# Kernel optimization log

Hardware: AMD Instinct MI355X
Metric: run time of the kernel (lower is better)

## Reference

```python
import jax, jax.numpy as jnp
import numpy as np

N, Fdim, Aout = 8192, 32, 8
AVG_DEG = 32.0  # target average degree for the random graph


def setup_inputs() -> dict:
    key = jax.random.key(0)
    ks = jax.random.split(key, 12)
    x = jax.random.normal(ks[0], (N, Fdim), dtype=jnp.float32)
    # binary adjacency, zero diagonal (GCNConv adds self-loops itself)
    u = jax.random.uniform(ks[1], (N, N), dtype=jnp.float32)
    adj = (u < (AVG_DEG / N)).astype(jnp.float32)
    adj = adj * (1.0 - jnp.eye(N, dtype=jnp.float32))
    mask = (jax.random.uniform(ks[2], (N,), dtype=jnp.float32) < 0.5).astype(jnp.float32)

    def lin(k, fout, fin):
        s = 1.0 / np.sqrt(fin)
        return jax.random.uniform(k, (fout, fin), jnp.float32, -s, s)

    return {
        "x": x, "adj": adj, "mask": mask,
        "w1": lin(ks[3], 64, Fdim), "b1": jnp.zeros((64,), jnp.float32),
        "w2": lin(ks[4], 128, 64), "b2": jnp.zeros((128,), jnp.float32),
        "wg": lin(ks[5], 128, 128), "bg": jnp.zeros((128,), jnp.float32),
        "wd": lin(ks[6], 128, 128), "bd": jnp.zeros((128,), jnp.float32),
        "wp1": lin(ks[7], 128, 256), "bp1": jnp.zeros((128,), jnp.float32),
        "wp2": lin(ks[8], 64, 128), "bp2": jnp.zeros((64,), jnp.float32),
        "wo": lin(ks[9], Aout, 64), "bo": jnp.zeros((Aout,), jnp.float32),
    }


def reference(x, adj, mask, w1, b1, w2, b2, wg, bg, wd, bd, wp1, bp1, wp2, bp2, wo, bo):
    # encoder MLP
    h = jax.nn.relu(x @ w1.T + b1)           # [N,64]
    h = jax.nn.relu(h @ w2.T + b2)           # [N,128]
    # GCNConv with default self-loops and symmetric normalization:
    # out = D^{-1/2} (A + I) D^{-1/2} (h W^T) + b
    a_hat = adj + jnp.eye(adj.shape[0], dtype=adj.dtype)
    deg = jnp.sum(a_hat, axis=1)             # >= 1 thanks to self-loops
    dinv = jax.lax.rsqrt(deg)
    msg = h @ wg.T                            # [N,128]
    agg = dinv[:, None] * (a_hat @ (dinv[:, None] * msg))  # normalized aggregation
    g = jax.nn.relu(agg + bg)
    g = jax.nn.relu(g @ wd.T + bd)
    f = jnp.concatenate([g, h], axis=1)       # [N,256]
    p = jax.nn.relu(f @ wp1.T + bp1)
    p = jax.nn.relu(p @ wp2.T + bp2)
    out = (p @ wo.T + bo) * mask[:, None]     # [N,Aout]
    return out
```

## Files before the change

kernel.cpp:

```cpp
#include <hip/hip_runtime.h>

#define N_NODES 8192
#define CAP 128
#define ETILE 16
constexpr int AST = 132;
constexpr int WST = 129;

#define GLDS16(gsrc, ldst)                                                      \
  __builtin_amdgcn_global_load_lds(                                             \
      (const __attribute__((address_space(1))) void*)(gsrc),                    \
      (__attribute__((address_space(3))) void*)(ldst), 16, 0, 0)

__global__ __launch_bounds__(256, 2) void scan_kernel(
    const float* __restrict__ adj, int* __restrict__ cnt,
    int* __restrict__ nbr) {
  __shared__ uint4 stage[4][2][512];
  const int t = threadIdx.x;
  const int lane = t & 63;
  const int w = t >> 6;
  const int row = blockIdx.x * 4 + w;
  const float* rowg = adj + (size_t)row * N_NODES;
  const unsigned long long lmask = (1ull << lane) - 1;

#pragma unroll
  for (int i = 0; i < 8; ++i)
    GLDS16(rowg + i * 256 + lane * 4, &stage[w][0][i * 64]);

  int running = 0;
  int* nbr_row = nbr + (size_t)row * CAP;
#pragma unroll
  for (int ch = 0; ch < 4; ++ch) {
    if (ch < 3) {
#pragma unroll
      for (int i = 0; i < 8; ++i)
        GLDS16(rowg + (ch + 1) * 2048 + i * 256 + lane * 4,
               &stage[w][(ch + 1) & 1][i * 64]);
      __builtin_amdgcn_s_waitcnt(0x3F78);
    } else {
      __builtin_amdgcn_s_waitcnt(0x3F70);
    }
    asm volatile("" ::: "memory");
    uint4 v[8];
#pragma unroll
    for (int i = 0; i < 8; ++i) v[i] = stage[w][ch & 1][i * 64 + lane];
    int c = 0;
#pragma unroll
    for (int i = 0; i < 8; ++i)
      c += (v[i].x != 0u) + (v[i].y != 0u) + (v[i].z != 0u) + (v[i].w != 0u);
    int incl = c;
#pragma unroll
    for (int s = 1; s < 64; s <<= 1) {
      int n = __shfl_up(incl, s);
      if (lane >= s) incl += n;
    }
    int off = running + incl - c;
    running += __shfl(incl, 63);
    const int colbase = ch * 2048;
#pragma unroll
    for (int i = 0; i < 8; ++i) {
      if (v[i].x | v[i].y | v[i].z | v[i].w) {
        const int col = colbase + (i * 64 + lane) * 4;
        if (v[i].x) { if (off < CAP) nbr_row[off] = col + 0; ++off; }
        if (v[i].y) { if (off < CAP) nbr_row[off] = col + 1; ++off; }
        if (v[i].z) { if (off < CAP) nbr_row[off] = col + 2; ++off; }
        if (v[i].w) { if (off < CAP) nbr_row[off] = col + 3; ++off; }
      }
    }
  }
  if (lane == 0) cnt[row] = running;
}

template <int TILE, int K, int KSPLIT, int F, bool RELU, bool BIAS, int SCALEMODE>
__device__ __forceinline__ void layer_op(
    const float (*__restrict__ A0)[AST], const float (*__restrict__ A1)[AST],
    float (*__restrict__ Aout)[AST], float (*__restrict__ Wb)[WST],
    const float* __restrict__ W, const float* __restrict__ bias,
    float* __restrict__ gout, const float* __restrict__ rowscale,
    const int* __restrict__ degcnt, int n0, int t) {
  constexpr int KC = 32;
  constexpr int NCH = K / KC;
  constexpr int ACT = (F * TILE < 256) ? F * TILE : 256;
  constexpr int RS = ACT / F;
  constexpr int RPT = TILE / RS;
  const int c = t % F;
  const int rb = t / F;
  float acc[RPT];
#pragma unroll
  for (int i = 0; i < RPT; ++i) acc[i] = 0.f;

  for (int ch = 0; ch < NCH; ++ch) {
#pragma unroll
    for (int i = 0; i < (F * KC + 255) / 256; ++i) {
      int lin = t + i * 256;
      if ((F * KC) % 256 == 0 || lin < F * KC) {
        int k = lin % KC, f = lin / KC;
        Wb[k][f] = W[(size_t)f * K + ch * KC + k];
      }
    }
    __syncthreads();
    if (t < ACT) {
      const float (*__restrict__ As)[AST] = (ch * KC < KSPLIT) ? A0 : A1;
      const int kb = (ch * KC < KSPLIT) ? ch * KC : ch * KC - KSPLIT;
#pragma unroll
      for (int kg = 0; kg < KC / 4; ++kg) {
        float w0 = Wb[kg * 4 + 0][c];
        float w1v = Wb[kg * 4 + 1][c];
        float w2v = Wb[kg * 4 + 2][c];
        float w3v = Wb[kg * 4 + 3][c];
#pragma unroll
        for (int i = 0; i < RPT; ++i) {
          const float4 a = *(const float4*)&As[rb + i * RS][kb + kg * 4];
          acc[i] = fmaf(a.x, w0, acc[i]);
          acc[i] = fmaf(a.y, w1v, acc[i]);
          acc[i] = fmaf(a.z, w2v, acc[i]);
          acc[i] = fmaf(a.w, w3v, acc[i]);
        }
      }
    }
    __syncthreads();
  }
  if (t < ACT) {
#pragma unroll
    for (int i = 0; i < RPT; ++i) {
      float v = acc[i];
      if (BIAS) v += bias[c];
      if (RELU) v = fmaxf(v, 0.f);
      int node = n0 + rb + i * RS;
      if (SCALEMODE == 1) v *= rowscale[node];
      if (SCALEMODE == 2) v *= rsqrtf((float)degcnt[node] + 1.0f);
      if (Aout) Aout[rb + i * RS][c] = v;
      if (gout) gout[(size_t)node * F + c] = v;
    }
  }
}

__global__ __launch_bounds__(256) void encode_kernel(
    const float* __restrict__ x,
    const float* __restrict__ w1, const float* __restrict__ b1,
    const float* __restrict__ w2, const float* __restrict__ b2,
    const float* __restrict__ wg, const int* __restrict__ cnt,
    float* __restrict__ h_out, float* __restrict__ msg_out) {
  __shared__ float bufA[ETILE][AST];
  __shared__ float bufB[ETILE][AST];
  __shared__ float Wb[32][WST];
  const int t = threadIdx.x;
  const int n0 = blockIdx.x * ETILE;
  if (t < 128) {
    int row = t >> 3, k4 = (t & 7) * 4;
    *(float4*)&bufA[row][k4] = *(const float4*)&x[(size_t)(n0 + row) * 32 + k4];
  }
  layer_op<ETILE, 32, 32, 64, true, true, 0>(bufA, nullptr, bufB, Wb, w1, b1, nullptr, nullptr, nullptr, n0, t);
  layer_op<ETILE, 64, 64, 128, true, true, 0>(bufB, nullptr, bufA, Wb, w2, b2, h_out, nullptr, nullptr, n0, t);
  layer_op<ETILE, 128, 128, 128, false, false, 2>(bufA, nullptr, nullptr, Wb, wg, nullptr, msg_out, nullptr, cnt, n0, t);
}

__global__ __launch_bounds__(256) void agg_kernel(
    const int* __restrict__ cnt, const int* __restrict__ nbr,
    const float* __restrict__ msg, const float* __restrict__ bg,
    const float* __restrict__ adj, float* __restrict__ g1) {
  const int t = threadIdx.x;
  const int f = t & 127;
  const int row = blockIdx.x * 2 + (t >> 7);
  float acc = msg[(size_t)row * 128 + f];
  const int c = cnt[row];
  const float dv = rsqrtf((float)c + 1.0f);
  if (c <= CAP) {
    int i = 0;
    for (; i + 4 <= c; i += 4) {
      int j0 = nbr[(size_t)row * CAP + i + 0];
      int j1 = nbr[(size_t)row * CAP + i + 1];
      int j2 = nbr[(size_t)row * CAP + i + 2];
      int j3 = nbr[(size_t)row * CAP + i + 3];
      float a0 = msg[(size_t)j0 * 128 + f];
      float a1 = msg[(size_t)j1 * 128 + f];
      float a2 = msg[(size_t)j2 * 128 + f];
      float a3 = msg[(size_t)j3 * 128 + f];
      acc += (a0 + a1) + (a2 + a3);
    }
    for (; i < c; ++i) {
      int j = nbr[(size_t)row * CAP + i];
      acc += msg[(size_t)j * 128 + f];
    }
  } else {
    acc = msg[(size_t)row * 128 + f];
    for (int col = 0; col < N_NODES; ++col) {
      if (adj[(size_t)row * N_NODES + col] != 0.f) acc += msg[(size_t)col * 128 + f];
    }
  }
  float v = fmaf(dv, acc, bg[f]);
  g1[(size_t)row * 128 + f] = fmaxf(v, 0.f);
}

__global__ __launch_bounds__(256) void decode_kernel(
    const float* __restrict__ g1, const float* __restrict__ h,
    const float* __restrict__ wd, const float* __restrict__ bd,
    const float* __restrict__ wp1, const float* __restrict__ bp1,
    const float* __restrict__ wp2, const float* __restrict__ bp2,
    const float* __restrict__ wo, const float* __restrict__ bo,
    const float* __restrict__ mask, float* __restrict__ out) {
  __shared__ float bufA[ETILE][AST];
  __shared__ float bufB[ETILE][AST];
  __shared__ float bufH[ETILE][AST];
  __shared__ float Wb[32][WST];
  const int t = threadIdx.x;
  const int n0 = blockIdx.x * ETILE;
#pragma unroll
  for (int i = 0; i < 2; ++i) {
    int lin = t + i * 256;
    int row = lin >> 5, k4 = (lin & 31) * 4;
    *(float4*)&bufA[row][k4] = *(const float4*)&g1[(size_t)(n0 + row) * 128 + k4];
    *(float4*)&bufH[row][k4] = *(const float4*)&h[(size_t)(n0 + row) * 128 + k4];
  }
  layer_op<ETILE, 128, 128, 128, true, true, 0>(bufA, nullptr, bufB, Wb, wd, bd, nullptr, nullptr, nullptr, n0, t);
  layer_op<ETILE, 256, 128, 128, true, true, 0>(bufB, bufH, bufA, Wb, wp1, bp1, nullptr, nullptr, nullptr, n0, t);
  layer_op<ETILE, 128, 128, 64, true, true, 0>(bufA, nullptr, bufB, Wb, wp2, bp2, nullptr, nullptr, nullptr, n0, t);
  layer_op<ETILE, 64, 64, 8, false, true, 1>(bufB, nullptr, nullptr, Wb, wo, bo, out, mask, nullptr, n0, t);
}

extern "C" void kernel_launch(void* const* d_in, const int* in_sizes, int n_in,
                              void* d_out, int out_size, void* d_ws, size_t ws_size,
                              hipStream_t stream) {
  const float* x    = (const float*)d_in[0];
  const float* adj  = (const float*)d_in[1];
  const float* mask = (const float*)d_in[2];
  const float* w1   = (const float*)d_in[3];
  const float* b1   = (const float*)d_in[4];
  const float* w2   = (const float*)d_in[5];
  const float* b2   = (const float*)d_in[6];
  const float* wg   = (const float*)d_in[7];
  const float* bg   = (const float*)d_in[8];
  const float* wd   = (const float*)d_in[9];
  const float* bd   = (const float*)d_in[10];
  const float* wp1  = (const float*)d_in[11];
  const float* bp1  = (const float*)d_in[12];
  const float* wp2  = (const float*)d_in[13];
  const float* bp2  = (const float*)d_in[14];
  const float* wo   = (const float*)d_in[15];
  const float* bo   = (const float*)d_in[16];
  float* out = (float*)d_out;

  float* ws = (float*)d_ws;
  float* h    = ws; ws += (size_t)N_NODES * 128;
  float* msg  = ws; ws += (size_t)N_NODES * 128;
  float* g1   = ws; ws += (size_t)N_NODES * 128;
  int* cnt = (int*)ws; ws += N_NODES;
  int* nbr = (int*)ws;

  scan_kernel<<<N_NODES / 4, 256, 0, stream>>>(adj, cnt, nbr);
  encode_kernel<<<N_NODES / ETILE, 256, 0, stream>>>(x, w1, b1, w2, b2, wg, cnt, h, msg);
  agg_kernel<<<N_NODES / 2, 256, 0, stream>>>(cnt, nbr, msg, bg, adj, g1);
  decode_kernel<<<N_NODES / ETILE, 256, 0, stream>>>(
      g1, h, wd, bd, wp1, bp1, wp2, bp2, wo, bo, mask, out);
}
```

Baseline: 465.2 us.

## Use register-prefetched nontemporal loads in scan, two rows per thread in agg, smaller decode tile

The adjacency scan drops the LDS-staged global_load_lds double buffer. It now prefetches the next chunk straight into registers with nontemporal loads, and the occupancy hint rises to 4 blocks per SM. The aggregation kernel handles two rows per thread with masked, clamped neighbor loads so more independent gathers are in flight, at the cost of some wasted loads when the two degrees differ. The decode kernel uses an 8-row tile, which doubles the block count and cuts LDS use per block but reuses each weight tile less.

```diff
diff --git a/kernel.cpp b/kernel.cpp
--- a/kernel.cpp
+++ b/kernel.cpp
@@ -3,46 +3,30 @@
 #define N_NODES 8192
 #define CAP 128
 #define ETILE 16
+#define DTILE 8
 constexpr int AST = 132;
 constexpr int WST = 129;
 
-#define GLDS16(gsrc, ldst)                                                      \
-  __builtin_amdgcn_global_load_lds(                                             \
-      (const __attribute__((address_space(1))) void*)(gsrc),                    \
-      (__attribute__((address_space(3))) void*)(ldst), 16, 0, 0)
-
-__global__ __launch_bounds__(256, 2) void scan_kernel(
+typedef unsigned u32x4 __attribute__((ext_vector_type(4)));
+
+__global__ __launch_bounds__(256, 4) void scan_kernel(
     const float* __restrict__ adj, int* __restrict__ cnt,
     int* __restrict__ nbr) {
-  __shared__ uint4 stage[4][2][512];
   const int t = threadIdx.x;
   const int lane = t & 63;
-  const int w = t >> 6;
-  const int row = blockIdx.x * 4 + w;
-  const float* rowg = adj + (size_t)row * N_NODES;
-  const unsigned long long lmask = (1ull << lane) - 1;
-
-#pragma unroll
-  for (int i = 0; i < 8; ++i)
-    GLDS16(rowg + i * 256 + lane * 4, &stage[w][0][i * 64]);
-
+  const int row = blockIdx.x * 4 + (t >> 6);
+  const u32x4* rowp = (const u32x4*)(adj + (size_t)row * N_NODES);
+  u32x4 v[8], vn[8];
+#pragma unroll
+  for (int i = 0; i < 8; ++i) v[i] = __builtin_nontemporal_load(&rowp[i * 64 + lane]);
   int running = 0;
   int* nbr_row = nbr + (size_t)row * CAP;
-#pragma unroll
   for (int ch = 0; ch < 4; ++ch) {
     if (ch < 3) {
-#pragma unroll
-      for (int i = 0; i < 8; ++i)
-        GLDS16(rowg + (ch + 1) * 2048 + i * 256 + lane * 4,
-               &stage[w][(ch + 1) & 1][i * 64]);
-      __builtin_amdgcn_s_waitcnt(0x3F78);
-    } else {
-      __builtin_amdgcn_s_waitcnt(0x3F70);
-    }
-    asm volatile("" ::: "memory");
-    uint4 v[8];
-#pragma unroll
-    for (int i = 0; i < 8; ++i) v[i] = stage[w][ch & 1][i * 64 + lane];
+      const u32x4* cp = rowp + (ch + 1) * 512;
+#pragma unroll
+      for (int i = 0; i < 8; ++i) vn[i] = __builtin_nontemporal_load(&cp[i * 64 + lane]);
+    }
     int c = 0;
 #pragma unroll
     for (int i = 0; i < 8; ++i)
@@ -66,6 +50,8 @@
         if (v[i].w) { if (off < CAP) nbr_row[off] = col + 3; ++off; }
       }
     }
+#pragma unroll
+    for (int i = 0; i < 8; ++i) v[i] = vn[i];
   }
   if (lane == 0) cnt[row] = running;
 }
@@ -160,35 +146,39 @@
     const float* __restrict__ adj, float* __restrict__ g1) {
   const int t = threadIdx.x;
   const int f = t & 127;
-  const int row = blockIdx.x * 2 + (t >> 7);
-  float acc = msg[(size_t)row * 128 + f];
-  const int c = cnt[row];
-  const float dv = rsqrtf((float)c + 1.0f);
-  if (c <= CAP) {
-    int i = 0;
-    for (; i + 4 <= c; i += 4) {
-      int j0 = nbr[(size_t)row * CAP + i + 0];
-      int j1 = nbr[(size_t)row * CAP + i + 1];
-      int j2 = nbr[(size_t)row * CAP + i + 2];
-      int j3 = nbr[(size_t)row * CAP + i + 3];
-      float a0 = msg[(size_t)j0 * 128 + f];
-      float a1 = msg[(size_t)j1 * 128 + f];
-      float a2 = msg[(size_t)j2 * 128 + f];
-      float a3 = msg[(size_t)j3 * 128 + f];
-      acc += (a0 + a1) + (a2 + a3);
-    }
-    for (; i < c; ++i) {
-      int j = nbr[(size_t)row * CAP + i];
-      acc += msg[(size_t)j * 128 + f];
+  const int rA = blockIdx.x * 4 + (t >> 7) * 2;
+  const int rB = rA + 1;
+  const int cA = cnt[rA], cB = cnt[rB];
+  float a0 = msg[(size_t)rA * 128 + f];
+  float a1 = msg[(size_t)rB * 128 + f];
+  if (cA <= CAP && cB <= CAP) {
+    const int* nA = nbr + (size_t)rA * CAP;
+    const int* nB = nbr + (size_t)rB * CAP;
+    const int cm = max(cA, cB);
+    for (int i = 0; i < cm; i += 4) {
+#pragma unroll
+      for (int k = 0; k < 4; ++k) {
+        const int ii = i + k;
+        int jA = nA[ii < cA ? ii : 0] & (N_NODES - 1);
+        int jB = nB[ii < cB ? ii : 0] & (N_NODES - 1);
+        float vA = msg[(size_t)jA * 128 + f];
+        float vB = msg[(size_t)jB * 128 + f];
+        a0 += (ii < cA) ? vA : 0.f;
+        a1 += (ii < cB) ? vB : 0.f;
+      }
     }
   } else {
-    acc = msg[(size_t)row * 128 + f];
+    a0 = msg[(size_t)rA * 128 + f];
+    a1 = msg[(size_t)rB * 128 + f];
     for (int col = 0; col < N_NODES; ++col) {
-      if (adj[(size_t)row * N_NODES + col] != 0.f) acc += msg[(size_t)col * 128 + f];
-    }
-  }
-  float v = fmaf(dv, acc, bg[f]);
-  g1[(size_t)row * 128 + f] = fmaxf(v, 0.f);
+      if (adj[(size_t)rA * N_NODES + col] != 0.f) a0 += msg[(size_t)col * 128 + f];
+      if (adj[(size_t)rB * N_NODES + col] != 0.f) a1 += msg[(size_t)col * 128 + f];
+    }
+  }
+  float o0 = fmaf(rsqrtf((float)cA + 1.0f), a0, bg[f]);
+  float o1 = fmaf(rsqrtf((float)cB + 1.0f), a1, bg[f]);
+  g1[(size_t)rA * 128 + f] = fmaxf(o0, 0.f);
+  g1[(size_t)rB * 128 + f] = fmaxf(o1, 0.f);
 }
 
 __global__ __launch_bounds__(256) void decode_kernel(
@@ -198,23 +188,21 @@
     const float* __restrict__ wp2, const float* __restrict__ bp2,
     const float* __restrict__ wo, const float* __restrict__ bo,
     const float* __restrict__ mask, float* __restrict__ out) {
-  __shared__ float bufA[ETILE][AST];
-  __shared__ float bufB[ETILE][AST];
-  __shared__ float bufH[ETILE][AST];
+  __shared__ float bufA[DTILE][AST];
+  __shared__ float bufB[DTILE][AST];
+  __shared__ float bufH[DTILE][AST];
   __shared__ float Wb[32][WST];
   const int t = threadIdx.x;
-  const int n0 = blockIdx.x * ETILE;
-#pragma unroll
-  for (int i = 0; i < 2; ++i) {
-    int lin = t + i * 256;
-    int row = lin >> 5, k4 = (lin & 31) * 4;
+  const int n0 = blockIdx.x * DTILE;
+  {
+    int row = t >> 5, k4 = (t & 31) * 4;
     *(float4*)&bufA[row][k4] = *(const float4*)&g1[(size_t)(n0 + row) * 128 + k4];
     *(float4*)&bufH[row][k4] = *(const float4*)&h[(size_t)(n0 + row) * 128 + k4];
   }
-  layer_op<ETILE, 128, 128, 128, true, true, 0>(bufA, nullptr, bufB, Wb, wd, bd, nullptr, nullptr, nullptr, n0, t);
-  layer_op<ETILE, 256, 128, 128, true, true, 0>(bufB, bufH, bufA, Wb, wp1, bp1, nullptr, nullptr, nullptr, n0, t);
-  layer_op<ETILE, 128, 128, 64, true, true, 0>(bufA, nullptr, bufB, Wb, wp2, bp2, nullptr, nullptr, nullptr, n0, t);
-  layer_op<ETILE, 64, 64, 8, false, true, 1>(bufB, nullptr, nullptr, Wb, wo, bo, out, mask, nullptr, n0, t);
+  layer_op<DTILE, 128, 128, 128, true, true, 0>(bufA, nullptr, bufB, Wb, wd, bd, nullptr, nullptr, nullptr, n0, t);
+  layer_op<DTILE, 256, 128, 128, true, true, 0>(bufB, bufH, bufA, Wb, wp1, bp1, nullptr, nullptr, nullptr, n0, t);
+  layer_op<DTILE, 128, 128, 64, true, true, 0>(bufA, nullptr, bufB, Wb, wp2, bp2, nullptr, nullptr, nullptr, n0, t);
+  layer_op<DTILE, 64, 64, 8, false, true, 1>(bufB, nullptr, nullptr, Wb, wo, bo, out, mask, nullptr, n0, t);
 }
 
 extern "C" void kernel_launch(void* const* d_in, const int* in_sizes, int n_in,
@@ -248,7 +236,7 @@
 
   scan_kernel<<<N_NODES / 4, 256, 0, stream>>>(adj, cnt, nbr);
   encode_kernel<<<N_NODES / ETILE, 256, 0, stream>>>(x, w1, b1, w2, b2, wg, cnt, h, msg);
-  agg_kernel<<<N_NODES / 2, 256, 0, stream>>>(cnt, nbr, msg, bg, adj, g1);
-  decode_kernel<<<N_NODES / ETILE, 256, 0, stream>>>(
+  agg_kernel<<<N_NODES / 4, 256, 0, stream>>>(cnt, nbr, msg, bg, adj, g1);
+  decode_kernel<<<N_NODES / DTILE, 256, 0, stream>>>(
       g1, h, wd, bd, wp1, bp1, wp2, bp2, wo, bo, mask, out);
 }
```

After: 455.3 us. -2.1%, faster.
